# Optimization experiments

Hardware: AMD Instinct MI355X
Metric: run time of the kernel (lower is better)

The kernel has to match this reference:

```python
import jax, jax.numpy as jnp
import numpy as np

N_PTS = 100000
C_IN, C_OUT, K = 16, 32, 3
B, D, H, W = 2, 32, 128, 128


def setup_inputs() -> dict:
    key = jax.random.key(0)
    kf, kw, kb, kz, ky, kx = jax.random.split(key, 6)
    features = jax.random.normal(kf, (N_PTS, C_IN), dtype=jnp.float32)
    coords = jnp.stack([
        jax.random.randint(kb, (N_PTS,), 0, B),
        jax.random.randint(kz, (N_PTS,), 0, D),
        jax.random.randint(ky, (N_PTS,), 0, H),
        jax.random.randint(kx, (N_PTS,), 0, W),
    ], axis=1).astype(jnp.int32)
    weight = jax.random.normal(kw, (K ** 3, C_IN, C_OUT), dtype=jnp.float32) * 0.01
    bias = jnp.zeros((C_OUT,), dtype=jnp.float32)
    return {"features": features, "coords": coords, "weight": weight, "bias": bias,
            "batch_size": B, "d_sp": D, "h_sp": H, "w_sp": W}


def reference(features, coords, weight, bias, batch_size, d_sp, h_sp, w_sp):
    # Scatter sparse voxel features into dense grid (B, C_in, D, H, W).
    n, c_in = features.shape
    c_out = weight.shape[2]
    k = K
    b, z, y, x = coords[:, 0], coords[:, 1], coords[:, 2], coords[:, 3]
    dense = jnp.zeros((batch_size, c_in, d_sp, h_sp, w_sp), dtype=features.dtype)
    dense = dense.at[b, :, z, y, x].set(features)  # (N,) advanced idx -> rows of (N, C_in)
    # Conv3d: torch copies weight.view(C_out, C_in, k, k, k) -> OIDHW kernel.
    kernel = weight.reshape(c_out, c_in, k, k, k)
    out = jax.lax.conv_general_dilated(
        dense, kernel,
        window_strides=(1, 1, 1),
        padding=[(1, 1), (1, 1), (1, 1)],
        dimension_numbers=("NCDHW", "OIDHW", "NCDHW"))
    out = jax.nn.relu(out + bias[None, :, None, None, None])
    # Dense equivalent of the torch nonzero-gather (which has data-dependent
    # shape): return the full dense activated grid (B, C_out, D, H, W).
    return out
```

## Files before the change

kernel.cpp:

```cpp
#include <hip/hip_runtime.h>

#define CIN   16
#define COUT  32
#define BATCH 2
#define DSP   32
#define HSP   128
#define WSP   128
#define NVOX  (BATCH*DSP*HSP*WSP)

#define DP (DSP+2)
#define HP (HSP+2)
#define WP (WSP+2)
#define ZSTR (HP*WP)
#define NVOXP (BATCH*DP*HP*WP)

#define TZ 4
#define TY 8
#define TX 32
#define NTZ 8
#define NTY 16
#define NTX 4
#define NTILES 1024
#define PZ 6
#define PYY 10
#define PXX 34
#define PVOX (PZ*PYY*PXX)
#define NCHUNK (2*PVOX)
#define NPAIR 14
#define NWREP ((NPAIR*2*64*8 + 255)/256)

typedef __bf16 bf16x8 __attribute__((ext_vector_type(8)));
typedef float  f32x4  __attribute__((ext_vector_type(4)));

__device__ __forceinline__ void load_lds16(const void* g, void* l) {
    __builtin_amdgcn_global_load_lds(
        (const __attribute__((address_space(1))) unsigned*)g,
        (__attribute__((address_space(3))) unsigned*)l, 16, 0, 0);
}

__global__ void k_prep(const int4* __restrict__ coords, int n, int nbDedup,
                       int* __restrict__ map,
                       const float* __restrict__ w, __bf16* __restrict__ wpack) {
    int bb = blockIdx.x;
    if (bb < nbDedup) {
        int p = bb * 256 + threadIdx.x;
        if (p >= n) return;
        int4 c = coords[p];
        int vox = ((c.x*DSP + c.y)*HSP + c.z)*WSP + c.w;
        atomicMax(&map[vox], p);
    } else {
        int i = (bb - nbDedup) * 256 + threadIdx.x;
        if (i >= NPAIR*2*64*8) return;
        int j = i & 7, l = (i>>3) & 63, h = (i>>9) & 1, p = i >> 10;
        int tap = 2*p + ((l>>4)>>1);
        int co  = h*16 + (l & 15);
        int ci  = ((l>>4)&1)*8 + j;
        float v = (tap < 27) ? w[(co*CIN + ci)*27 + tap] : 0.0f;
        wpack[i] = (__bf16)v;
    }
}

__global__ void k_scatter(const int4* __restrict__ coords, const int* __restrict__ map,
                          const float* __restrict__ feat, __bf16* __restrict__ dense,
                          int n) {
    int p = blockIdx.x * 256 + threadIdx.x;
    if (p >= n) return;
    int4 c = coords[p];
    int vox = ((c.x*DSP + c.y)*HSP + c.z)*WSP + c.w;
    if (map[vox] != p) return;
    const float4* fp = (const float4*)(feat + (size_t)p*CIN);
    float4 f0 = fp[0], f1 = fp[1], f2 = fp[2], f3 = fp[3];
    bf16x8 lo = { (__bf16)f0.x,(__bf16)f0.y,(__bf16)f0.z,(__bf16)f0.w,
                  (__bf16)f1.x,(__bf16)f1.y,(__bf16)f1.z,(__bf16)f1.w };
    bf16x8 hi = { (__bf16)f2.x,(__bf16)f2.y,(__bf16)f2.z,(__bf16)f2.w,
                  (__bf16)f3.x,(__bf16)f3.y,(__bf16)f3.z,(__bf16)f3.w };
    size_t voxp = (((size_t)c.x*DP + (c.y+1))*HP + (c.z+1))*WP + (c.w+1);
    __bf16* d = dense + voxp*CIN;
    *(bf16x8*)d       = lo;
    *(bf16x8*)(d + 8) = hi;
}

__global__ __launch_bounds__(512, 4) void k_conv(
    const __bf16* __restrict__ dense, const __bf16* __restrict__ wpack,
    const float* __restrict__ bias, float* __restrict__ out)
{
    __shared__ __align__(16) ushort patch[NCHUNK*8];

    int bid  = blockIdx.x;
    int tile = (bid & 7) * (NTILES/8) + (bid >> 3);
    int txi = tile & 3;
    int tyi = (tile >> 2) & 15;
    int tzi = (tile >> 6) & 7;
    int b   = tile >> 9;
    int z0 = tzi*TZ, y0 = tyi*TY, x0 = txi*TX;

    int tid  = threadIdx.x;
    int lane = tid & 63, wave = tid >> 6;

    const __bf16* gbase = dense + ((((size_t)b*DP + z0)*HP + y0)*WP + x0)*CIN;
    for (int j0 = wave*64; j0 < NCHUNK; j0 += 512) {
        int j = j0 + lane;
        if (j < NCHUNK) {
            int h  = (j >= PVOX) ? 1 : 0;
            int v  = j - h*PVOX;
            int pz = v / (PYY*PXX);
            int rem = v - pz*(PYY*PXX);
            int py = rem / PXX;
            int px = rem - py*PXX;
            load_lds16(gbase + ((size_t)(pz*ZSTR + py*WP + px))*CIN + h*8,
                       (void*)(patch + (size_t)j0*8));
        }
    }

    int lx16  = lane & 15;
    int lhalf = (lane >> 4) & 1;
    int ltp   = (lane >> 4) >> 1;
    int zw    = wave >> 1;
    int yb    = (wave & 1) * 4;

    int voff[NPAIR];
    #pragma unroll
    for (int p = 0; p < NPAIR; ++p) {
        int tap = 2*p + ltp; if (tap > 26) tap = 26;
        int kd = tap/9, kh = (tap/3)%3, kw = tap%3;
        voff[p] = (kd*PYY + kh)*PXX + kw;
    }
    float bv0 = bias[lx16], bv1 = bias[16 + lx16];

    __syncthreads();

    f32x4 acc[8][2];
    #pragma unroll
    for (int gi = 0; gi < 8; ++gi) {
        acc[gi][0] = (f32x4){0.f,0.f,0.f,0.f};
        acc[gi][1] = (f32x4){0.f,0.f,0.f,0.f};
    }
    const ushort* pb = patch + ((size_t)lhalf*PVOX + (zw*PYY + yb)*PXX + lx16)*8;
    bf16x8 w0 = *(const bf16x8*)(wpack + (size_t)(0*64 + lane)*8);
    bf16x8 w1 = *(const bf16x8*)(wpack + (size_t)(1*64 + lane)*8);
    #pragma unroll
    for (int p = 0; p < NPAIR; ++p) {
        int pn = (p + 1 < NPAIR) ? p + 1 : 0;
        bf16x8 nw0 = *(const bf16x8*)(wpack + (size_t)((pn*2+0)*64 + lane)*8);
        bf16x8 nw1 = *(const bf16x8*)(wpack + (size_t)((pn*2+1)*64 + lane)*8);
        const ushort* pa = pb + (size_t)voff[p]*8;
        #pragma unroll
        for (int gi = 0; gi < 8; ++gi) {
            bf16x8 a = *(const bf16x8*)(pa + ((gi>>1)*PXX + (gi&1)*16)*8);
            acc[gi][0] = __builtin_amdgcn_mfma_f32_16x16x32_bf16(a, w0, acc[gi][0], 0,0,0);
            acc[gi][1] = __builtin_amdgcn_mfma_f32_16x16x32_bf16(a, w1, acc[gi][1], 0,0,0);
        }
        w0 = nw0; w1 = nw1;
    }

    #pragma unroll
    for (int gi = 0; gi < 8; ++gi) {
        int y = yb + (gi >> 1), xg = gi & 1;
        int gz = z0 + zw, gy = y0 + y, gx = x0 + xg*16 + ((lane >> 4) << 2);
        f32x4 o0, o1;
        o0[0] = fmaxf(acc[gi][0][0]+bv0, 0.f); o0[1] = fmaxf(acc[gi][0][1]+bv0, 0.f);
        o0[2] = fmaxf(acc[gi][0][2]+bv0, 0.f); o0[3] = fmaxf(acc[gi][0][3]+bv0, 0.f);
        o1[0] = fmaxf(acc[gi][1][0]+bv1, 0.f); o1[1] = fmaxf(acc[gi][1][1]+bv1, 0.f);
        o1[2] = fmaxf(acc[gi][1][2]+bv1, 0.f); o1[3] = fmaxf(acc[gi][1][3]+bv1, 0.f);
        size_t base0 = ((((size_t)b*COUT + lx16)*DSP + gz)*HSP + gy)*WSP + gx;
        size_t base1 = base0 + (size_t)16*DSP*HSP*WSP;
        *(f32x4*)(out + base0) = o0;
        *(f32x4*)(out + base1) = o1;
    }
}

extern "C" void kernel_launch(void* const* d_in, const int* in_sizes, int n_in,
                              void* d_out, int out_size, void* d_ws, size_t ws_size,
                              hipStream_t stream) {
    const float* feat   = (const float*)d_in[0];
    const int4*  coords = (const int4*)d_in[1];
    const float* weight = (const float*)d_in[2];
    const float* bias   = (const float*)d_in[3];
    float* out = (float*)d_out;
    int n = in_sizes[0] / CIN;

    int*    map   = (int*)d_ws;
    __bf16* dense = (__bf16*)(map + NVOX);
    __bf16* wpack = dense + (size_t)NVOXP*CIN;

    hipMemsetAsync(map, 0xFF, (size_t)NVOX*sizeof(int), stream);
    hipMemsetAsync(dense, 0, (size_t)NVOXP*CIN*sizeof(__bf16), stream);

    int nb = (n + 255) / 256;
    k_prep   <<<nb + NWREP, 256, 0, stream>>>(coords, n, nb, map, weight, wpack);
    k_scatter<<<nb, 256, 0, stream>>>(coords, map, feat, dense, n);
    k_conv   <<<NTILES, 512, 0, stream>>>(dense, wpack, bias, out);
}
```

Before: 83.33 us.

## Double-buffer conv tiles along x and fold dense zeroing into prep kernel

Each conv block now handles four x-tiles in sequence instead of one. While computing the current tile it loads the next tile into a second LDS buffer, and it keeps all weight fragments in registers for the whole block. The dense-grid memset is replaced by extra blocks in the prep kernel, which removes one separate launch. The grid drops to 256 blocks and launch bounds to 2 blocks per CU, so the kernel trades occupancy and register pressure for overlap of global loads with MFMA work and for reusing the weight loads.

Measured after the change: 82.66 us. About the same (-0.8%).

```diff
diff --git a/kernel.cpp b/kernel.cpp
--- a/kernel.cpp
+++ b/kernel.cpp
@@ -17,17 +17,17 @@
 #define TZ 4
 #define TY 8
 #define TX 32
-#define NTZ 8
-#define NTY 16
-#define NTX 4
-#define NTILES 1024
 #define PZ 6
 #define PYY 10
 #define PXX 34
-#define PVOX (PZ*PYY*PXX)
+#define PROW (PYY*PXX)
+#define PVOX (PZ*PROW)
 #define NCHUNK (2*PVOX)
+#define NCHPAD 4096
 #define NPAIR 14
 #define NWREP ((NPAIR*2*64*8 + 255)/256)
+#define FILLT (NVOXP*CIN/8)
+#define NFILL ((FILLT + 255)/256)
 
 typedef __bf16 bf16x8 __attribute__((ext_vector_type(8)));
 typedef float  f32x4  __attribute__((ext_vector_type(4)));
@@ -40,7 +40,8 @@
 
 __global__ void k_prep(const int4* __restrict__ coords, int n, int nbDedup,
                        int* __restrict__ map,
-                       const float* __restrict__ w, __bf16* __restrict__ wpack) {
+                       const float* __restrict__ w, __bf16* __restrict__ wpack,
+                       uint4* __restrict__ dense4) {
     int bb = blockIdx.x;
     if (bb < nbDedup) {
         int p = bb * 256 + threadIdx.x;
@@ -48,7 +49,7 @@
         int4 c = coords[p];
         int vox = ((c.x*DSP + c.y)*HSP + c.z)*WSP + c.w;
         atomicMax(&map[vox], p);
-    } else {
+    } else if (bb < nbDedup + NWREP) {
         int i = (bb - nbDedup) * 256 + threadIdx.x;
         if (i >= NPAIR*2*64*8) return;
         int j = i & 7, l = (i>>3) & 63, h = (i>>9) & 1, p = i >> 10;
@@ -57,6 +58,9 @@
         int ci  = ((l>>4)&1)*8 + j;
         float v = (tap < 27) ? w[(co*CIN + ci)*27 + tap] : 0.0f;
         wpack[i] = (__bf16)v;
+    } else {
+        int i = (bb - nbDedup - NWREP) * 256 + threadIdx.x;
+        if (i < FILLT) dense4[i] = make_uint4(0,0,0,0);
     }
 }
 
@@ -80,38 +84,37 @@
     *(bf16x8*)(d + 8) = hi;
 }
 
-__global__ __launch_bounds__(512, 4) void k_conv(
+__device__ __forceinline__ void stage_tile(const __bf16* __restrict__ gb,
+                                           ushort* lbase, int wave, int lane) {
+    #pragma unroll
+    for (int it = 0; it < 8; ++it) {
+        int j0 = wave*64 + it*512;
+        int j  = j0 + lane;
+        int jj = j < NCHUNK ? j : NCHUNK-1;
+        int h  = (jj >= PVOX) ? 1 : 0;
+        int v  = jj - h*PVOX;
+        int pz = v / PROW;
+        int rem = v - pz*PROW;
+        int py = rem / PXX;
+        int px = rem - py*PXX;
+        load_lds16(gb + ((size_t)(pz*ZSTR + py*WP + px))*CIN + h*8,
+                   (void*)(lbase + (size_t)j0*8));
+    }
+}
+
+__global__ __launch_bounds__(512, 2) void k_conv(
     const __bf16* __restrict__ dense, const __bf16* __restrict__ wpack,
     const float* __restrict__ bias, float* __restrict__ out)
 {
-    __shared__ __align__(16) ushort patch[NCHUNK*8];
-
-    int bid  = blockIdx.x;
-    int tile = (bid & 7) * (NTILES/8) + (bid >> 3);
-    int txi = tile & 3;
-    int tyi = (tile >> 2) & 15;
-    int tzi = (tile >> 6) & 7;
-    int b   = tile >> 9;
-    int z0 = tzi*TZ, y0 = tyi*TY, x0 = txi*TX;
+    __shared__ __align__(16) ushort patch[2][NCHPAD*8];
+
+    int bid = blockIdx.x;
+    int bs  = (bid & 7) * 32 + (bid >> 3);
+    int tyi = bs & 15, tzi = (bs >> 4) & 7, b = bs >> 7;
+    int z0 = tzi*TZ, y0 = tyi*TY;
 
     int tid  = threadIdx.x;
     int lane = tid & 63, wave = tid >> 6;
-
-    const __bf16* gbase = dense + ((((size_t)b*DP + z0)*HP + y0)*WP + x0)*CIN;
-    for (int j0 = wave*64; j0 < NCHUNK; j0 += 512) {
-        int j = j0 + lane;
-        if (j < NCHUNK) {
-            int h  = (j >= PVOX) ? 1 : 0;
-            int v  = j - h*PVOX;
-            int pz = v / (PYY*PXX);
-            int rem = v - pz*(PYY*PXX);
-            int py = rem / PXX;
-            int px = rem - py*PXX;
-            load_lds16(gbase + ((size_t)(pz*ZSTR + py*WP + px))*CIN + h*8,
-                       (void*)(patch + (size_t)j0*8));
-        }
-    }
-
     int lx16  = lane & 15;
     int lhalf = (lane >> 4) & 1;
     int ltp   = (lane >> 4) >> 1;
@@ -127,45 +130,64 @@
     }
     float bv0 = bias[lx16], bv1 = bias[16 + lx16];
 
-    __syncthreads();
-
-    f32x4 acc[8][2];
+    bf16x8 wf[NPAIR][2];
     #pragma unroll
-    for (int gi = 0; gi < 8; ++gi) {
-        acc[gi][0] = (f32x4){0.f,0.f,0.f,0.f};
-        acc[gi][1] = (f32x4){0.f,0.f,0.f,0.f};
-    }
-    const ushort* pb = patch + ((size_t)lhalf*PVOX + (zw*PYY + yb)*PXX + lx16)*8;
-    bf16x8 w0 = *(const bf16x8*)(wpack + (size_t)(0*64 + lane)*8);
-    bf16x8 w1 = *(const bf16x8*)(wpack + (size_t)(1*64 + lane)*8);
-    #pragma unroll
-    for (int p = 0; p < NPAIR; ++p) {
-        int pn = (p + 1 < NPAIR) ? p + 1 : 0;
-        bf16x8 nw0 = *(const bf16x8*)(wpack + (size_t)((pn*2+0)*64 + lane)*8);
-        bf16x8 nw1 = *(const bf16x8*)(wpack + (size_t)((pn*2+1)*64 + lane)*8);
-        const ushort* pa = pb + (size_t)voff[p]*8;
+    for (int p = 0; p < NPAIR; ++p)
+        #pragma unroll
+        for (int h = 0; h < 2; ++h)
+            wf[p][h] = *(const bf16x8*)(wpack + (size_t)((p*2 + h)*64 + lane)*8);
+
+    const __bf16* grow = dense + ((((size_t)b*DP + z0)*HP + y0)*WP)*CIN;
+
+    stage_tile(grow, patch[0], wave, lane);
+
+    #pragma unroll 1
+    for (int t = 0; t < 4; ++t) {
+        if (t < 3) {
+            stage_tile(grow + (size_t)(t+1)*TX*CIN, patch[(t+1)&1], wave, lane);
+            asm volatile("s_waitcnt vmcnt(8)\ns_barrier" ::: "memory");
+        } else {
+            asm volatile("s_waitcnt vmcnt(0)\ns_barrier" ::: "memory");
+        }
+        __builtin_amdgcn_sched_barrier(0);
+
+        f32x4 acc[8][2];
         #pragma unroll
         for (int gi = 0; gi < 8; ++gi) {
-            bf16x8 a = *(const bf16x8*)(pa + ((gi>>1)*PXX + (gi&1)*16)*8);
-            acc[gi][0] = __builtin_amdgcn_mfma_f32_16x16x32_bf16(a, w0, acc[gi][0], 0,0,0);
-            acc[gi][1] = __builtin_amdgcn_mfma_f32_16x16x32_bf16(a, w1, acc[gi][1], 0,0,0);
-        }
-        w0 = nw0; w1 = nw1;
-    }
-
-    #pragma unroll
-    for (int gi = 0; gi < 8; ++gi) {
-        int y = yb + (gi >> 1), xg = gi & 1;
-        int gz = z0 + zw, gy = y0 + y, gx = x0 + xg*16 + ((lane >> 4) << 2);
-        f32x4 o0, o1;
-        o0[0] = fmaxf(acc[gi][0][0]+bv0, 0.f); o0[1] = fmaxf(acc[gi][0][1]+bv0, 0.f);
-        o0[2] = fmaxf(acc[gi][0][2]+bv0, 0.f); o0[3] = fmaxf(acc[gi][0][3]+bv0, 0.f);
-        o1[0] = fmaxf(acc[gi][1][0]+bv1, 0.f); o1[1] = fmaxf(acc[gi][1][1]+bv1, 0.f);
-        o1[2] = fmaxf(acc[gi][1][2]+bv1, 0.f); o1[3] = fmaxf(acc[gi][1][3]+bv1, 0.f);
-        size_t base0 = ((((size_t)b*COUT + lx16)*DSP + gz)*HSP + gy)*WSP + gx;
-        size_t base1 = base0 + (size_t)16*DSP*HSP*WSP;
-        *(f32x4*)(out + base0) = o0;
-        *(f32x4*)(out + base1) = o1;
+            acc[gi][0] = (f32x4){0.f,0.f,0.f,0.f};
+            acc[gi][1] = (f32x4){0.f,0.f,0.f,0.f};
+        }
+        const ushort* pb = patch[t&1] +
+            ((size_t)lhalf*PVOX + (zw*PYY + yb)*PXX + lx16)*8;
+        #pragma unroll
+        for (int p = 0; p < NPAIR; ++p) {
+            const ushort* pa = pb + (size_t)voff[p]*8;
+            #pragma unroll
+            for (int gi = 0; gi < 8; ++gi) {
+                bf16x8 a = *(const bf16x8*)(pa + ((gi>>1)*PXX + (gi&1)*16)*8);
+                acc[gi][0] = __builtin_amdgcn_mfma_f32_16x16x32_bf16(a, wf[p][0], acc[gi][0], 0,0,0);
+                acc[gi][1] = __builtin_amdgcn_mfma_f32_16x16x32_bf16(a, wf[p][1], acc[gi][1], 0,0,0);
+            }
+        }
+
+        asm volatile("s_barrier" ::: "memory");
+        __builtin_amdgcn_sched_barrier(0);
+
+        #pragma unroll
+        for (int gi = 0; gi < 8; ++gi) {
+            int y = yb + (gi >> 1), xg = gi & 1;
+            int gz = z0 + zw, gy = y0 + y;
+            int gx = t*TX + xg*16 + ((lane >> 4) << 2);
+            f32x4 o0, o1;
+            o0[0] = fmaxf(acc[gi][0][0]+bv0, 0.f); o0[1] = fmaxf(acc[gi][0][1]+bv0, 0.f);
+            o0[2] = fmaxf(acc[gi][0][2]+bv0, 0.f); o0[3] = fmaxf(acc[gi][0][3]+bv0, 0.f);
+            o1[0] = fmaxf(acc[gi][1][0]+bv1, 0.f); o1[1] = fmaxf(acc[gi][1][1]+bv1, 0.f);
+            o1[2] = fmaxf(acc[gi][1][2]+bv1, 0.f); o1[3] = fmaxf(acc[gi][1][3]+bv1, 0.f);
+            size_t base0 = ((((size_t)b*COUT + lx16)*DSP + gz)*HSP + gy)*WSP + gx;
+            size_t base1 = base0 + (size_t)16*DSP*HSP*WSP;
+            *(f32x4*)(out + base0) = o0;
+            *(f32x4*)(out + base1) = o1;
+        }
     }
 }
 
@@ -184,10 +206,10 @@
     __bf16* wpack = dense + (size_t)NVOXP*CIN;
 
     hipMemsetAsync(map, 0xFF, (size_t)NVOX*sizeof(int), stream);
-    hipMemsetAsync(dense, 0, (size_t)NVOXP*CIN*sizeof(__bf16), stream);
 
     int nb = (n + 255) / 256;
-    k_prep   <<<nb + NWREP, 256, 0, stream>>>(coords, n, nb, map, weight, wpack);
+    k_prep   <<<nb + NWREP + NFILL, 256, 0, stream>>>(coords, n, nb, map, weight,
+                                                      wpack, (uint4*)dense);
     k_scatter<<<nb, 256, 0, stream>>>(coords, map, feat, dense, n);
-    k_conv   <<<NTILES, 512, 0, stream>>>(dense, wpack, bias, out);
-}
+    k_conv   <<<256, 512, 0, stream>>>(dense, wpack, bias, out);
+}
```
